# Kernel tuning notes

Measured on AMD Instinct MI355X. Metric: run time of the kernel, lower is better.

Reference implementation:

```python
import jax, jax.numpy as jnp
import numpy as np

NUM_HEADS = 16
D_MODEL = 1024
D_K = D_MODEL // NUM_HEADS


def setup_inputs() -> dict:
    key = jax.random.key(0)
    ks = jax.random.split(key, 12)
    B, S = 2, 2048
    scale = 1.0 / np.sqrt(D_MODEL)
    inp = {
        "query": jax.random.normal(ks[0], (B, S, D_MODEL), jnp.float32),
        "key": jax.random.normal(ks[1], (B, S, D_MODEL), jnp.float32),
        "value": jax.random.normal(ks[2], (B, S, D_MODEL), jnp.float32),
        "mask": jnp.ones((B, S, S), jnp.int32),
        "Wq": jax.random.normal(ks[3], (D_MODEL, D_MODEL), jnp.float32) * scale,
        "bq": jax.random.normal(ks[4], (D_MODEL,), jnp.float32) * scale,
        "Wk": jax.random.normal(ks[5], (D_MODEL, D_MODEL), jnp.float32) * scale,
        "bk": jax.random.normal(ks[6], (D_MODEL,), jnp.float32) * scale,
        "Wv": jax.random.normal(ks[7], (D_MODEL, D_MODEL), jnp.float32) * scale,
        "bv": jax.random.normal(ks[8], (D_MODEL,), jnp.float32) * scale,
        "Wo": jax.random.normal(ks[9], (D_MODEL, D_MODEL), jnp.float32) * scale,
        "bo": jax.random.normal(ks[10], (D_MODEL,), jnp.float32) * scale,
    }
    return inp


def _split_heads(x):
    B, S, _ = x.shape
    return x.reshape(B, S, NUM_HEADS, D_K).transpose(0, 2, 1, 3)  # [B,H,S,d_k]


def reference(query, key, value, mask, Wq, bq, Wk, bk, Wv, bv, Wo, bo):
    # torch Linear: y = x @ W.T + b
    q = _split_heads(query @ Wq.T + bq)
    k = _split_heads(key @ Wk.T + bk)
    v = _split_heads(value @ Wv.T + bv)
    scores = jnp.einsum("bhqd,bhkd->bhqk", q, k) / np.sqrt(D_K)
    scores = jnp.where(mask[:, None, :, :] == 0, jnp.float32(-1e9), scores)
    p_attn = jax.nn.softmax(scores, axis=-1)
    attn = jnp.einsum("bhqk,bhkd->bhqd", p_attn, v)  # [B,H,S,d_k]
    B, _, S, _ = attn.shape
    x = attn.transpose(0, 2, 1, 3).reshape(B, S, D_MODEL)
    return x @ Wo.T + bo
```

## Files before the change

kernel.cpp:

```cpp
#include <hip/hip_runtime.h>
#include <hip/hip_bf16.h>
#include <cstdint>

#define DEVINL static __device__ __forceinline__

typedef __attribute__((ext_vector_type(4))) float floatx4;
typedef __attribute__((ext_vector_type(8))) short bf16x8;

DEVINL unsigned short f2bf(float f) {
    union { float f; uint32_t u; } v; v.f = f;
    return (unsigned short)((v.u + 0x7FFFu + ((v.u >> 16) & 1u)) >> 16);
}

DEVINL uint32_t pk2bf(float x, float y) {
    __hip_bfloat162 h = __float22bfloat162_rn(float2{x, y});
    union { __hip_bfloat162 h; uint32_t u; } v; v.h = h;
    return v.u;
}

DEVINL floatx4 mfma16(bf16x8 a, bf16x8 b, floatx4 c) {
    return __builtin_amdgcn_mfma_f32_16x16x32_bf16(a, b, c, 0, 0, 0);
}

#define GLDS16(g, l)                                                            \
    __builtin_amdgcn_global_load_lds(                                           \
        (const __attribute__((address_space(1))) void*)(g),                     \
        (__attribute__((address_space(3))) void*)(l), 16, 0, 0)

constexpr int B_ = 2, S_ = 2048, D_ = 1024, H_ = 16, DK_ = 64;
constexpr int BSROWS = B_ * S_;
constexpr int NQB = S_ / 128;
constexpr int NKT = S_ / 64;

constexpr float QSCALE = 0.18033688011112042f;

__device__ int g_flags[B_ * NQB * NKT];

__global__ __launch_bounds__(256)
void prep(const float* __restrict__ q, const float* __restrict__ k,
          const float* __restrict__ v,
          const float* __restrict__ Wq, const float* __restrict__ Wk,
          const float* __restrict__ Wv, const float* __restrict__ Wo,
          unsigned short* __restrict__ qb, unsigned short* __restrict__ kb,
          unsigned short* __restrict__ vb,
          unsigned short* __restrict__ wqb, unsigned short* __restrict__ wkb,
          unsigned short* __restrict__ wvb, unsigned short* __restrict__ wob,
          const int* __restrict__ mask)
{
    __shared__ int f;
    int bid = blockIdx.x;
    if (bid < 8192) {
        const float* src; unsigned short* dst; int rb;
        if      (bid < 2048) { src = q;  dst = qb;  rb = bid; }
        else if (bid < 4096) { src = k;  dst = kb;  rb = bid - 2048; }
        else if (bid < 6144) { src = v;  dst = vb;  rb = bid - 4096; }
        else if (bid < 6656) { src = Wq; dst = wqb; rb = bid - 6144; }
        else if (bid < 7168) { src = Wk; dst = wkb; rb = bid - 6656; }
        else if (bid < 7680) { src = Wv; dst = wvb; rb = bid - 7168; }
        else                 { src = Wo; dst = wob; rb = bid - 7680; }
        size_t e = ((size_t)rb * 256 + threadIdx.x) * 8;
        float4 v0 = *(const float4*)(src + e);
        float4 v1 = *(const float4*)(src + e + 4);
        uint4 o;
        o.x = pk2bf(v0.x, v0.y); o.y = pk2bf(v0.z, v0.w);
        o.z = pk2bf(v1.x, v1.y); o.w = pk2bf(v1.z, v1.w);
        *(uint4*)(dst + e) = o;
    } else {
        int mb = bid - 8192;
        int kt = mb & 31, qq = (mb >> 5) & 15, b = mb >> 9;
        const int* base = mask + (size_t)(b * S_ + qq * 128) * S_ + kt * 64;
        int ok = 1;
        #pragma unroll
        for (int i = 0; i < 8; ++i) {
            int u = threadIdx.x + 256 * i;
            int row = u >> 4, c = u & 15;
            int4 m = *(const int4*)(base + (size_t)row * S_ + c * 4);
            if ((m.x == 0) | (m.y == 0) | (m.z == 0) | (m.w == 0)) ok = 0;
        }
        if (threadIdx.x == 0) f = 1;
        __syncthreads();
        if (!ok) f = 0;
        __syncthreads();
        if (threadIdx.x == 0) g_flags[mb] = f;
    }
}

__global__ __launch_bounds__(256)
void gemm_qkv(const unsigned short* __restrict__ qb, const unsigned short* __restrict__ kb,
              const unsigned short* __restrict__ vb,
              const unsigned short* __restrict__ wqb, const unsigned short* __restrict__ wkb,
              const unsigned short* __restrict__ wvb,
              const float* __restrict__ bq, const float* __restrict__ bk,
              const float* __restrict__ bv,
              unsigned short* __restrict__ Qp, unsigned short* __restrict__ KpF,
              unsigned short* __restrict__ VpF)
{
    constexpr int K = D_, N = D_;
    __shared__ unsigned short As[2][128 * 64];
    __shared__ unsigned short Wss[2][64 * 64];

    const int bid = blockIdx.x;
    const int xcd = bid & 7, sl = bid >> 3;
    const int z = sl >> 6, rr = sl & 63;
    const int nb = rr >> 2, mloc = rr & 3;
    const int m0 = (mloc * 8 + xcd) * 128, n0 = nb * 64;

    const unsigned short* A = z == 0 ? qb  : z == 1 ? kb  : vb;
    const unsigned short* W = z == 0 ? wqb : z == 1 ? wkb : wvb;
    const float* bias       = z == 0 ? bq  : z == 1 ? bk  : bv;

    const int tid  = threadIdx.x;
    const int lane = tid & 63, wave = tid >> 6;
    const int lr = lane & 15, lg = lane >> 4;
    const int wm = (wave >> 1) * 64, wn = (wave & 1) * 32;

    int rowA[4], kcA[4], rowW[2], kcW[2];
    #pragma unroll
    for (int j = 0; j < 4; ++j) {
        int L = (wave * 4 + j) * 64 + lane;
        rowA[j] = L >> 3; kcA[j] = (L & 7) ^ (rowA[j] & 7);
    }
    #pragma unroll
    for (int j = 0; j < 2; ++j) {
        int L = (wave * 2 + j) * 64 + lane;
        rowW[j] = L >> 3; kcW[j] = (L & 7) ^ (rowW[j] & 7);
    }

    auto dma = [&](int k0, int buf) {
        #pragma unroll
        for (int j = 0; j < 4; ++j)
            GLDS16(A + (size_t)(m0 + rowA[j]) * K + k0 + kcA[j] * 8,
                   &As[buf][(wave * 4 + j) * 512 + lane * 8]);
        #pragma unroll
        for (int j = 0; j < 2; ++j)
            GLDS16(W + (size_t)(n0 + rowW[j]) * K + k0 + kcW[j] * 8,
                   &Wss[buf][(wave * 2 + j) * 512 + lane * 8]);
    };

    floatx4 acc[4][2];
    #pragma unroll
    for (int mt = 0; mt < 4; ++mt)
        #pragma unroll
        for (int nt = 0; nt < 2; ++nt)
            acc[mt][nt] = floatx4{0.f, 0.f, 0.f, 0.f};

    dma(0, 0);
    for (int it = 0; it < K / 64; ++it) {
        __syncthreads();
        if (it + 1 < K / 64) dma((it + 1) * 64, (it + 1) & 1);
        const int buf = it & 1;

        #pragma unroll
        for (int kf = 0; kf < 2; ++kf) {
            bf16x8 af[4], bfr[2];
            #pragma unroll
            for (int mt = 0; mt < 4; ++mt) {
                int row = wm + mt * 16 + lr;
                af[mt] = *(const bf16x8*)&As[buf][row * 64 + (((kf * 4 + lg) ^ (lr & 7)) * 8)];
            }
            #pragma unroll
            for (int nt = 0; nt < 2; ++nt) {
                int row = wn + nt * 16 + lr;
                bfr[nt] = *(const bf16x8*)&Wss[buf][row * 64 + (((kf * 4 + lg) ^ (lr & 7)) * 8)];
            }
            #pragma unroll
            for (int mt = 0; mt < 4; ++mt)
                #pragma unroll
                for (int nt = 0; nt < 2; ++nt)
                    acc[mt][nt] = mfma16(af[mt], bfr[nt], acc[mt][nt]);
        }
    }

    if (z == 0) {
        #pragma unroll
        for (int nt = 0; nt < 2; ++nt) {
            int col = n0 + wn + nt * 16 + lr;
            float bv2 = bias[col];
            #pragma unroll
            for (int mt = 0; mt < 4; ++mt)
                #pragma unroll
                for (int reg = 0; reg < 4; ++reg) {
                    int row = m0 + wm + mt * 16 + lg * 4 + reg;
                    Qp[(size_t)row * N + col] = f2bf((acc[mt][nt][reg] + bv2) * QSCALE);
                }
        }
    } else if (z == 1) {
        #pragma unroll
        for (int nt = 0; nt < 2; ++nt) {
            int c = n0 + wn + nt * 16 + lr;
            int h = c >> 6, d = c & 63;
            int kfA = d >> 5, lgA = (d >> 3) & 3, j = d & 7;
            float bv2 = bias[c];
            #pragma unroll
            for (int mt = 0; mt < 4; ++mt)
                #pragma unroll
                for (int reg = 0; reg < 4; ++reg) {
                    int t = m0 + wm + mt * 16 + lg * 4 + reg;
                    int bb = t >> 11, sx = t & (S_ - 1);
                    int kt = sx >> 6, key = sx & 63;
                    int mtA = key >> 4, lrA = key & 15;
                    size_t off = (((size_t)(bb * 16 + h) * 32 + kt) * 8 + (kfA * 4 + mtA)) * 512
                               + (lrA + 16 * lgA) * 8 + j;
                    KpF[off] = f2bf(acc[mt][nt][reg] + bv2);
                }
        }
    } else {
        #pragma unroll
        for (int nt = 0; nt < 2; ++nt) {
            int c = n0 + wn + nt * 16 + lr;
            int h = c >> 6, dtA = (c >> 4) & 3;
            float bv2 = bias[c];
            #pragma unroll
            for (int mt = 0; mt < 4; ++mt) {
                int t0 = m0 + wm + mt * 16 + lg * 4;
                int bb = t0 >> 11, s0 = t0 & (S_ - 1);
                int kt = s0 >> 6, key = s0 & 63;
                int kfA = key >> 5, lgA = (key >> 3) & 3, j0 = key & 7;
                size_t off = (((size_t)(bb * 16 + h) * 32 + kt) * 8 + (dtA * 2 + kfA)) * 512
                           + (lr + 16 * lgA) * 8 + j0;
                uint2 p;
                p.x = pk2bf(acc[mt][nt][0] + bv2, acc[mt][nt][1] + bv2);
                p.y = pk2bf(acc[mt][nt][2] + bv2, acc[mt][nt][3] + bv2);
                *(uint2*)&VpF[off] = p;
            }
        }
    }
}

__global__ __launch_bounds__(256, 2)
void attn_flash(const unsigned short* __restrict__ Qp,
                const unsigned short* __restrict__ KpF,
                const unsigned short* __restrict__ VpF,
                const int* __restrict__ mask,
                unsigned short* __restrict__ Out)
{
    constexpr int LD = 72;
    __shared__ unsigned short Ps[128 * LD];

    const int tid = threadIdx.x;
    const int lane = tid & 63, wave = tid >> 6;
    const int lr = lane & 15, lg = lane >> 4;
    const int h = blockIdx.x, qb = blockIdx.y, b = blockIdx.z;
    const int q0 = qb * 128, qw = q0 + wave * 32;

    bf16x8 qf[2][2];
    #pragma unroll
    for (int qt = 0; qt < 2; ++qt)
        #pragma unroll
        for (int kf = 0; kf < 2; ++kf)
            qf[qt][kf] = *(const bf16x8*)(Qp + (size_t)(b * S_ + qw + qt * 16 + lr) * D_ +
                                          h * DK_ + kf * 32 + lg * 8);

    float l_[2] = {0.f, 0.f};
    floatx4 o_acc[2][4];
    #pragma unroll
    for (int qt = 0; qt < 2; ++qt)
        #pragma unroll
        for (int dt = 0; dt < 4; ++dt) o_acc[qt][dt] = floatx4{0.f, 0.f, 0.f, 0.f};

    const unsigned short* kbase = KpF + (size_t)(b * 16 + h) * 32 * 4096 + lane * 8;
    const unsigned short* vbase = VpF + (size_t)(b * 16 + h) * 32 * 4096 + lane * 8;
    const int fbase = (b * NQB + qb) * NKT;
    unsigned short* PsW = &Ps[(wave * 32 + lr) * LD];

    auto loadKV = [&](int kt, bf16x8 (&kfr)[8], bf16x8 (&vfr)[8]) {
        const unsigned short* kb = kbase + kt * 4096;
        const unsigned short* vb = vbase + kt * 4096;
        #pragma unroll
        for (int c = 0; c < 8; ++c) kfr[c] = *(const bf16x8*)(kb + c * 512);
        #pragma unroll
        for (int c = 0; c < 8; ++c) vfr[c] = *(const bf16x8*)(vb + c * 512);
    };

    auto process = [&](int kt, bf16x8 (&kfr)[8], bf16x8 (&vfr)[8]) {
        floatx4 sc[2][4];
        #pragma unroll
        for (int qt = 0; qt < 2; ++qt)
            #pragma unroll
            for (int mt = 0; mt < 4; ++mt) sc[qt][mt] = floatx4{0.f, 0.f, 0.f, 0.f};
        #pragma unroll
        for (int mt = 0; mt < 4; ++mt)
            #pragma unroll
            for (int kf = 0; kf < 2; ++kf)
                #pragma unroll
                for (int qt = 0; qt < 2; ++qt)
                    sc[qt][mt] = mfma16(kfr[kf * 4 + mt], qf[qt][kf], sc[qt][mt]);

        if (g_flags[fbase + kt] == 0) {
            #pragma unroll
            for (int qt = 0; qt < 2; ++qt) {
                int qq = qw + qt * 16 + lr;
                const int* mrow = mask + (size_t)(b * S_ + qq) * S_ + kt * 64;
                #pragma unroll
                for (int mt = 0; mt < 4; ++mt)
                    #pragma unroll
                    for (int reg = 0; reg < 4; ++reg)
                        if (mrow[mt * 16 + lg * 4 + reg] == 0)
                            sc[qt][mt][reg] = -1e9f;
            }
        }

        #pragma unroll
        for (int qt = 0; qt < 2; ++qt) {
            #pragma unroll
            for (int mt = 0; mt < 4; ++mt) {
                float p0 = __builtin_amdgcn_exp2f(sc[qt][mt][0]);
                float p1 = __builtin_amdgcn_exp2f(sc[qt][mt][1]);
                float p2 = __builtin_amdgcn_exp2f(sc[qt][mt][2]);
                float p3 = __builtin_amdgcn_exp2f(sc[qt][mt][3]);
                l_[qt] += (p0 + p1) + (p2 + p3);
                uint2 pk; pk.x = pk2bf(p0, p1); pk.y = pk2bf(p2, p3);
                *(uint2*)&PsW[qt * 16 * LD + mt * 16 + lg * 4] = pk;
            }
        }

        bf16x8 pb[2][2];
        #pragma unroll
        for (int qt = 0; qt < 2; ++qt)
            #pragma unroll
            for (int kf = 0; kf < 2; ++kf)
                pb[qt][kf] = *(const bf16x8*)&PsW[qt * 16 * LD + kf * 32 + lg * 8];
        #pragma unroll
        for (int dt = 0; dt < 4; ++dt)
            #pragma unroll
            for (int kf = 0; kf < 2; ++kf)
                #pragma unroll
                for (int qt = 0; qt < 2; ++qt)
                    o_acc[qt][dt] = mfma16(vfr[dt * 2 + kf], pb[qt][kf], o_acc[qt][dt]);
    };

    bf16x8 kA[8], vA[8], kB[8], vB[8];
    loadKV(0, kA, vA);
    for (int kt = 0; kt < NKT; kt += 2) {
        loadKV(kt + 1, kB, vB);
        process(kt, kA, vA);
        if (kt + 2 < NKT) loadKV(kt + 2, kA, vA);
        process(kt + 1, kB, vB);
    }

    #pragma unroll
    for (int qt = 0; qt < 2; ++qt) {
        float l = l_[qt];
        l += __shfl_xor(l, 16, 64);
        l += __shfl_xor(l, 32, 64);
        float inv = 1.f / l;
        int qq = qw + qt * 16 + lr;
        #pragma unroll
        for (int dt = 0; dt < 4; ++dt) {
            uint2 p;
            p.x = pk2bf(o_acc[qt][dt][0] * inv, o_acc[qt][dt][1] * inv);
            p.y = pk2bf(o_acc[qt][dt][2] * inv, o_acc[qt][dt][3] * inv);
            *(uint2*)&Out[(size_t)(b * S_ + qq) * D_ + h * DK_ + dt * 16 + lg * 4] = p;
        }
    }
}

__global__ __launch_bounds__(256)
void gemm_out(const unsigned short* __restrict__ Ap,
              const unsigned short* __restrict__ Wb,
              const float* __restrict__ bias, float* __restrict__ Cptr)
{
    constexpr int K = D_, N = D_;
    __shared__ unsigned short As[2][128 * 64];
    __shared__ unsigned short Wss[2][64 * 64];

    const int bid = blockIdx.x;
    const int xcd = bid & 7, sl = bid >> 3;
    const int nb = sl >> 2, mloc = sl & 3;
    const int m0 = (mloc * 8 + xcd) * 128, n0 = nb * 64;

    const int tid  = threadIdx.x;
    const int lane = tid & 63, wave = tid >> 6;
    const int lr = lane & 15, lg = lane >> 4;
    const int wm = (wave >> 1) * 64, wn = (wave & 1) * 32;

    int rowA[4], kcA[4], rowW[2], kcW[2];
    #pragma unroll
    for (int j = 0; j < 4; ++j) {
        int L = (wave * 4 + j) * 64 + lane;
        rowA[j] = L >> 3; kcA[j] = (L & 7) ^ (rowA[j] & 7);
    }
    #pragma unroll
    for (int j = 0; j < 2; ++j) {
        int L = (wave * 2 + j) * 64 + lane;
        rowW[j] = L >> 3; kcW[j] = (L & 7) ^ (rowW[j] & 7);
    }

    auto dma = [&](int k0, int buf) {
        #pragma unroll
        for (int j = 0; j < 4; ++j)
            GLDS16(Ap + (size_t)(m0 + rowA[j]) * K + k0 + kcA[j] * 8,
                   &As[buf][(wave * 4 + j) * 512 + lane * 8]);
        #pragma unroll
        for (int j = 0; j < 2; ++j)
            GLDS16(Wb + (size_t)(n0 + rowW[j]) * K + k0 + kcW[j] * 8,
                   &Wss[buf][(wave * 2 + j) * 512 + lane * 8]);
    };

    floatx4 acc[4][2];
    #pragma unroll
    for (int mt = 0; mt < 4; ++mt)
        #pragma unroll
        for (int nt = 0; nt < 2; ++nt)
            acc[mt][nt] = floatx4{0.f, 0.f, 0.f, 0.f};

    dma(0, 0);
    for (int it = 0; it < K / 64; ++it) {
        __syncthreads();
        if (it + 1 < K / 64) dma((it + 1) * 64, (it + 1) & 1);
        const int buf = it & 1;

        #pragma unroll
        for (int kf = 0; kf < 2; ++kf) {
            bf16x8 af[4], bfr[2];
            #pragma unroll
            for (int mt = 0; mt < 4; ++mt) {
                int row = wm + mt * 16 + lr;
                af[mt] = *(const bf16x8*)&As[buf][row * 64 + (((kf * 4 + lg) ^ (lr & 7)) * 8)];
            }
            #pragma unroll
            for (int nt = 0; nt < 2; ++nt) {
                int row = wn + nt * 16 + lr;
                bfr[nt] = *(const bf16x8*)&Wss[buf][row * 64 + (((kf * 4 + lg) ^ (lr & 7)) * 8)];
            }
            #pragma unroll
            for (int mt = 0; mt < 4; ++mt)
                #pragma unroll
                for (int nt = 0; nt < 2; ++nt)
                    acc[mt][nt] = mfma16(af[mt], bfr[nt], acc[mt][nt]);
        }
    }

    #pragma unroll
    for (int nt = 0; nt < 2; ++nt) {
        int col = n0 + wn + nt * 16 + lr;
        float bv2 = bias[col];
        #pragma unroll
        for (int mt = 0; mt < 4; ++mt)
            #pragma unroll
            for (int reg = 0; reg < 4; ++reg) {
                int row = m0 + wm + mt * 16 + lg * 4 + reg;
                Cptr[(size_t)row * N + col] = acc[mt][nt][reg] + bv2;
            }
    }
}

extern "C" void kernel_launch(void* const* d_in, const int* in_sizes, int n_in,
                              void* d_out, int out_size, void* d_ws, size_t ws_size,
                              hipStream_t stream)
{
    const float* query = (const float*)d_in[0];
    const float* key   = (const float*)d_in[1];
    const float* value = (const float*)d_in[2];
    const int*   mask  = (const int*)d_in[3];
    const float* Wq = (const float*)d_in[4];
    const float* bq = (const float*)d_in[5];
    const float* Wk = (const float*)d_in[6];
    const float* bk = (const float*)d_in[7];
    const float* Wv = (const float*)d_in[8];
    const float* bv = (const float*)d_in[9];
    const float* Wo = (const float*)d_in[10];
    const float* bo = (const float*)d_in[11];

    unsigned short* qb  = (unsigned short*)d_ws;
    unsigned short* kb  = qb  + (size_t)BSROWS * D_;
    unsigned short* vb  = kb  + (size_t)BSROWS * D_;
    unsigned short* wqb = vb  + (size_t)BSROWS * D_;
    unsigned short* wkb = wqb + (size_t)D_ * D_;
    unsigned short* wvb = wkb + (size_t)D_ * D_;
    unsigned short* wob = wvb + (size_t)D_ * D_;
    unsigned short* Qp  = wob + (size_t)D_ * D_;
    unsigned short* KpF = Qp  + (size_t)BSROWS * D_;
    unsigned short* VpF = KpF + (size_t)BSROWS * D_;
    unsigned short* Ap  = qb;

    dim3 blk(256);

    hipLaunchKernelGGL(prep, dim3(8192 + 1024), blk, 0, stream,
                       query, key, value, Wq, Wk, Wv, Wo,
                       qb, kb, vb, wqb, wkb, wvb, wob, mask);

    hipLaunchKernelGGL(gemm_qkv, dim3(1536), blk, 0, stream,
                       qb, kb, vb, wqb, wkb, wvb, bq, bk, bv, Qp, KpF, VpF);

    dim3 gattn(H_, NQB, B_);
    hipLaunchKernelGGL(attn_flash, gattn, blk, 0, stream, Qp, KpF, VpF, mask, Ap);

    hipLaunchKernelGGL(gemm_out, dim3(512), blk, 0, stream, Ap, wob, bo, (float*)d_out);
}
```

Before: 253.9 us.

## Stage K/V tiles cooperatively in double-buffered LDS via global-to-LDS loads

Previously each of the four waves loaded the full K and V tile for every key block straight into registers. That meant four redundant global reads per tile and four register-resident fragment sets for the two-deep prefetch. Now the block splits each tile's load across the waves, issuing direct global-to-LDS copies into a double-buffered shared array. Each wave then reads its fragments from LDS, which cuts global and L2 traffic and register pressure. In exchange it adds a block-wide barrier per key tile, extra LDS reads, and about 32KB more shared memory per block, which could limit occupancy.

```diff
diff --git a/kernel.cpp b/kernel.cpp
--- a/kernel.cpp
+++ b/kernel.cpp
@@ -236,6 +236,8 @@
 {
     constexpr int LD = 72;
     __shared__ unsigned short Ps[128 * LD];
+    __shared__ unsigned short Kt[2][4096];
+    __shared__ unsigned short Vt[2][4096];
 
     const int tid = threadIdx.x;
     const int lane = tid & 63, wave = tid >> 6;
@@ -258,21 +260,33 @@
         #pragma unroll
         for (int dt = 0; dt < 4; ++dt) o_acc[qt][dt] = floatx4{0.f, 0.f, 0.f, 0.f};
 
-    const unsigned short* kbase = KpF + (size_t)(b * 16 + h) * 32 * 4096 + lane * 8;
-    const unsigned short* vbase = VpF + (size_t)(b * 16 + h) * 32 * 4096 + lane * 8;
+    const unsigned short* ktile = KpF + (size_t)(b * 16 + h) * 32 * 4096;
+    const unsigned short* vtile = VpF + (size_t)(b * 16 + h) * 32 * 4096;
     const int fbase = (b * NQB + qb) * NKT;
     unsigned short* PsW = &Ps[(wave * 32 + lr) * LD];
 
-    auto loadKV = [&](int kt, bf16x8 (&kfr)[8], bf16x8 (&vfr)[8]) {
-        const unsigned short* kb = kbase + kt * 4096;
-        const unsigned short* vb = vbase + kt * 4096;
-        #pragma unroll
-        for (int c = 0; c < 8; ++c) kfr[c] = *(const bf16x8*)(kb + c * 512);
-        #pragma unroll
-        for (int c = 0; c < 8; ++c) vfr[c] = *(const bf16x8*)(vb + c * 512);
+    auto dmaKV = [&](int kt, int buf) {
+        const unsigned short* ks = ktile + kt * 4096;
+        const unsigned short* vs = vtile + kt * 4096;
+        #pragma unroll
+        for (int j = 0; j < 2; ++j) {
+            int g = wave * 2 + j;
+            GLDS16(ks + g * 512 + lane * 8, &Kt[buf][g * 512 + lane * 8]);
+            GLDS16(vs + g * 512 + lane * 8, &Vt[buf][g * 512 + lane * 8]);
+        }
     };
 
-    auto process = [&](int kt, bf16x8 (&kfr)[8], bf16x8 (&vfr)[8]) {
+    dmaKV(0, 0);
+    for (int kt = 0; kt < NKT; ++kt) {
+        __syncthreads();
+        if (kt + 1 < NKT) dmaKV(kt + 1, (kt + 1) & 1);
+        const int buf = kt & 1;
+
+        bf16x8 kfr[8];
+        #pragma unroll
+        for (int c = 0; c < 8; ++c)
+            kfr[c] = *(const bf16x8*)&Kt[buf][c * 512 + lane * 8];
+
         floatx4 sc[2][4];
         #pragma unroll
         for (int qt = 0; qt < 2; ++qt)
@@ -320,6 +334,11 @@
             #pragma unroll
             for (int kf = 0; kf < 2; ++kf)
                 pb[qt][kf] = *(const bf16x8*)&PsW[qt * 16 * LD + kf * 32 + lg * 8];
+
+        bf16x8 vfr[8];
+        #pragma unroll
+        for (int c = 0; c < 8; ++c)
+            vfr[c] = *(const bf16x8*)&Vt[buf][c * 512 + lane * 8];
         #pragma unroll
         for (int dt = 0; dt < 4; ++dt)
             #pragma unroll
@@ -327,15 +346,6 @@
                 #pragma unroll
                 for (int qt = 0; qt < 2; ++qt)
                     o_acc[qt][dt] = mfma16(vfr[dt * 2 + kf], pb[qt][kf], o_acc[qt][dt]);
-    };
-
-    bf16x8 kA[8], vA[8], kB[8], vB[8];
-    loadKV(0, kA, vA);
-    for (int kt = 0; kt < NKT; kt += 2) {
-        loadKV(kt + 1, kB, vB);
-        process(kt, kA, vA);
-        if (kt + 2 < NKT) loadKV(kt + 2, kA, vA);
-        process(kt + 1, kB, vB);
     }
 
     #pragma unroll
```

New measurement: 258.2 us. No clear change (+1.7%).
